# Kernel tuning notes

Measured on AMD Instinct MI355X. Metric: run time of the kernel, lower is better.

Reference implementation:

```python
import jax, jax.numpy as jnp
import numpy as np
from jax import lax

DIM = 2048
N_HEADS = 16
N_KV = 4
HEAD_DIM = DIM // N_HEADS  # 128
ROPE_BASE = 10000.0
SEQ = 4096
BSZ = 1


def bitlinear(x, W):
    # per-row abs-mean scale (detached), ternary round/clamp, straight-through blend
    s = lax.stop_gradient(jnp.clip(jnp.mean(jnp.abs(W), axis=1, keepdims=True), 1e-5, None))
    wt = jnp.clip(jnp.round(W / s), -1.0, 1.0)
    w = lax.stop_gradient(wt - W) + W  # straight-through
    return x @ (w * s).T


def rms_norm(x):
    eps = jnp.finfo(x.dtype).eps
    return x * lax.rsqrt(jnp.mean(x * x, axis=-1, keepdims=True) + eps)


def rope(x, cos, sin):
    half = x.shape[-1] // 2
    x1, x2 = x[..., :half], x[..., half:]
    return jnp.concatenate((x1 * cos + x2 * sin, -x1 * sin + x2 * cos), axis=-1)


def setup_inputs() -> dict:
    key = jax.random.key(0)
    ks = jax.random.split(key, 6)
    kv_dim = N_KV * HEAD_DIM
    return {
        "x": jax.random.normal(ks[0], (BSZ, SEQ, DIM), dtype=jnp.float32),
        "wq": jax.random.normal(ks[1], (DIM, DIM), dtype=jnp.float32) * 0.02,
        "wk": jax.random.normal(ks[2], (kv_dim, DIM), dtype=jnp.float32) * 0.02,
        "wv": jax.random.normal(ks[3], (kv_dim, DIM), dtype=jnp.float32) * 0.02,
        "wp": jax.random.normal(ks[4], (DIM, DIM), dtype=jnp.float32) * 0.02,
        "q_gain": jnp.ones((N_HEADS,), dtype=jnp.float32),
    }


def reference(x, wq, wk, wv, wp, q_gain):
    b, s, d = x.shape
    q = bitlinear(x, wq).reshape(b, s, N_HEADS, HEAD_DIM).transpose(0, 2, 1, 3)  # bhsd
    k = bitlinear(x, wk).reshape(b, s, N_KV, HEAD_DIM).transpose(0, 2, 1, 3)
    v = bitlinear(x, wv).reshape(b, s, N_KV, HEAD_DIM).transpose(0, 2, 1, 3)

    q = rms_norm(q)
    k = rms_norm(k)

    inv_freq = 1.0 / ROPE_BASE ** (jnp.arange(0, HEAD_DIM, 2, dtype=jnp.float32) / HEAD_DIM)
    t = jnp.arange(s, dtype=jnp.float32)
    freqs = jnp.outer(t, inv_freq)  # [s, hd/2]
    cos = jnp.cos(freqs)[None, None].astype(q.dtype)
    sin = jnp.sin(freqs)[None, None].astype(q.dtype)
    q = rope(q, cos, sin)
    k = rope(k, cos, sin)

    q = q * q_gain.astype(q.dtype)[None, :, None, None]

    groups = N_HEADS // N_KV
    k = jnp.repeat(k, groups, axis=1)  # GQA expand to [b, H, s, hd]
    v = jnp.repeat(v, groups, axis=1)

    scale = 1.0 / np.sqrt(HEAD_DIM)
    scores = jnp.einsum("bhqd,bhkd->bhqk", q, k) * scale
    causal = jnp.tril(jnp.ones((s, s), dtype=bool))
    scores = jnp.where(causal[None, None], scores, jnp.finfo(scores.dtype).min)
    attn = jax.nn.softmax(scores, axis=-1)
    y = jnp.einsum("bhqk,bhkd->bhqd", attn, v)

    y = y.transpose(0, 2, 1, 3).reshape(b, s, d)
    return bitlinear(y, wp)
```

## Files before the change

### kernel.cpp

```cpp
#include <hip/hip_runtime.h>
#include <math.h>

typedef unsigned short u16;
typedef short s16x8 __attribute__((ext_vector_type(8)));
typedef short s16x4 __attribute__((ext_vector_type(4)));
typedef float f32x4 __attribute__((ext_vector_type(4)));
typedef u16 u16x4 __attribute__((ext_vector_type(4)));

static constexpr size_t OFF_XB   = 0;
static constexpr size_t OFF_WQKV = 16777216;
static constexpr size_t OFF_WP   = 29360128;
static constexpr size_t OFF_QKV  = 37748736;
static constexpr size_t OFF_PART = 37748736 + 16777216;
static constexpr size_t OFF_KH   = 88080384;
static constexpr size_t OFF_VT   = 92274688;

__device__ __forceinline__ u16 f2bf(float f) {
  union { float f; unsigned u; } v; v.f = f;
  unsigned r = v.u + 0x7fffu + ((v.u >> 16) & 1u);
  return (u16)(r >> 16);
}

__device__ __forceinline__ void async16(const u16* g, u16* lds) {
  __builtin_amdgcn_global_load_lds(
      (const __attribute__((address_space(1))) void*)g,
      (__attribute__((address_space(3))) void*)lds, 16, 0, 0);
}

__global__ __launch_bounds__(256) void quant_rows(const float* __restrict__ W,
                                                  u16* __restrict__ out) {
  const int row = blockIdx.x, tid = threadIdx.x;
  const float* src = W + (size_t)row * 2048 + tid * 8;
  float4 a = *(const float4*)(src);
  float4 b = *(const float4*)(src + 4);
  float asum = fabsf(a.x)+fabsf(a.y)+fabsf(a.z)+fabsf(a.w)
             + fabsf(b.x)+fabsf(b.y)+fabsf(b.z)+fabsf(b.w);
  #pragma unroll
  for (int off = 1; off < 64; off <<= 1) asum += __shfl_xor(asum, off, 64);
  __shared__ float red[4];
  if ((tid & 63) == 0) red[tid >> 6] = asum;
  __syncthreads();
  float s = fmaxf((red[0]+red[1]+red[2]+red[3]) * (1.0f/2048.0f), 1e-5f);
  float v[8] = {a.x,a.y,a.z,a.w,b.x,b.y,b.z,b.w};
  u16* dst = out + (size_t)row * 2048 + tid * 8;
  #pragma unroll
  for (int i = 0; i < 8; i++) {
    float q = rintf(v[i] / s);
    q = fminf(fmaxf(q, -1.f), 1.f);
    dst[i] = f2bf(q * s);
  }
}

__global__ __launch_bounds__(256) void cvt_bf16(const float* __restrict__ in,
                                                u16* __restrict__ out) {
  size_t i = ((size_t)blockIdx.x * 256 + threadIdx.x) * 4;
  float4 v = *(const float4*)(in + i);
  u16x4 o;
  o.x = f2bf(v.x); o.y = f2bf(v.y); o.z = f2bf(v.z); o.w = f2bf(v.w);
  *(u16x4*)(out + i) = o;
}

__global__ __launch_bounds__(256) void gemm_bt(const u16* __restrict__ A,
                                               const u16* __restrict__ B,
                                               float* __restrict__ C,
                                               int M, int N, int K) {
  __shared__ u16 sA[128 * 32];
  __shared__ u16 sB[128 * 32];
  const int tid = threadIdx.x;
  const int lane = tid & 63;
  const int wid = tid >> 6;
  const int lr = lane & 15, lq = lane >> 4;
  const int wm = (wid >> 1) * 64, wn = (wid & 1) * 64;
  const size_t m0 = (size_t)blockIdx.y * 128, n0 = (size_t)blockIdx.x * 128;

  const int r0 = tid >> 2, c0 = (tid & 3) * 8;
  const u16* Ab0 = A + (m0 + r0) * (size_t)K + c0;
  const u16* Ab1 = A + (m0 + 64 + r0) * (size_t)K + c0;
  const u16* Bb0 = B + (n0 + r0) * (size_t)K + c0;
  const u16* Bb1 = B + (n0 + 64 + r0) * (size_t)K + c0;
  u16* sA0 = &sA[tid * 8];
  u16* sA1 = &sA[(256 + tid) * 8];
  u16* sB0 = &sB[tid * 8];
  u16* sB1 = &sB[(256 + tid) * 8];

  f32x4 acc[4][4] = {};

  for (int kt = 0; kt < K; kt += 32) {
    async16(Ab0 + kt, sA0);
    async16(Ab1 + kt, sA1);
    async16(Bb0 + kt, sB0);
    async16(Bb1 + kt, sB1);
    __syncthreads();
    s16x8 af[4], bf[4];
    #pragma unroll
    for (int mt = 0; mt < 4; mt++)
      af[mt] = *(const s16x8*)&sA[(wm + mt * 16 + lr) * 32 + lq * 8];
    #pragma unroll
    for (int nt = 0; nt < 4; nt++)
      bf[nt] = *(const s16x8*)&sB[(wn + nt * 16 + lr) * 32 + lq * 8];
    #pragma unroll
    for (int mt = 0; mt < 4; mt++)
      #pragma unroll
      for (int nt = 0; nt < 4; nt++)
        acc[mt][nt] = __builtin_amdgcn_mfma_f32_16x16x32_bf16(af[mt], bf[nt], acc[mt][nt], 0, 0, 0);
    __syncthreads();
  }
  #pragma unroll
  for (int mt = 0; mt < 4; mt++)
    #pragma unroll
    for (int nt = 0; nt < 4; nt++)
      #pragma unroll
      for (int r = 0; r < 4; r++) {
        size_t m = m0 + wm + mt * 16 + lq * 4 + r;
        size_t n = n0 + wn + nt * 16 + lr;
        C[m * (size_t)N + n] = acc[mt][nt][r];
      }
}

__global__ __launch_bounds__(256) void prep_qk(const float* __restrict__ qkv,
                                               const float* __restrict__ qgain,
                                               u16* __restrict__ Qh,
                                               u16* __restrict__ Kh) {
  const int s = blockIdx.y;
  const int j = blockIdx.x * 4 + (threadIdx.x >> 6);
  const int t = threadIdx.x & 63;
  const float* row = qkv + (size_t)s * 3072 + (size_t)j * 128;
  float x1 = row[t], x2 = row[t + 64];
  float ss = x1 * x1 + x2 * x2;
  #pragma unroll
  for (int off = 1; off < 64; off <<= 1) ss += __shfl_xor(ss, off, 64);
  float rn = rsqrtf(ss * (1.0f / 128.0f) + 1.1920929e-07f);
  float invf = exp2f(-(float)t * 0.20762050593048096f);
  float ang = (float)s * invf;
  float sn, c;
  sincosf(ang, &sn, &c);
  if (j < 16) {
    float g = qgain[j] * 0.12751738f;
    float q1 = x1 * rn, q2 = x2 * rn;
    float o1 = (q1 * c + q2 * sn) * g;
    float o2 = (-q1 * sn + q2 * c) * g;
    u16* dst = Qh + ((size_t)j * 4096 + s) * 128;
    dst[t] = f2bf(o1); dst[t + 64] = f2bf(o2);
  } else {
    float k1 = x1 * rn, k2 = x2 * rn;
    float o1 = k1 * c + k2 * sn;
    float o2 = -k1 * sn + k2 * c;
    u16* dst = Kh + ((size_t)(j - 16) * 4096 + s) * 128;
    dst[t] = f2bf(o1); dst[t + 64] = f2bf(o2);
  }
}

__global__ __launch_bounds__(256) void vtrans(const float* __restrict__ qkv,
                                              u16* __restrict__ Vtg) {
  __shared__ float tile[64][67];
  const int tid = threadIdx.x;
  const int s0 = blockIdx.y * 64;
  const int c0 = blockIdx.x * 64;
  #pragma unroll
  for (int it = 0; it < 4; it++) {
    int i = it * 256 + tid;
    int r = i >> 4, c = (i & 15) * 4;
    float4 v = *(const float4*)(qkv + (size_t)(s0 + r) * 3072 + 2560 + c0 + c);
    tile[r][c] = v.x; tile[r][c + 1] = v.y; tile[r][c + 2] = v.z; tile[r][c + 3] = v.w;
  }
  __syncthreads();
  #pragma unroll
  for (int it = 0; it < 2; it++) {
    int i = it * 256 + tid;
    int dl = i >> 3, sc = (i & 7) * 8;
    s16x8 ov;
    #pragma unroll
    for (int jj = 0; jj < 8; jj++) ov[jj] = (short)f2bf(tile[sc + jj][dl]);
    *(s16x8*)&Vtg[(size_t)(c0 + dl) * 4096 + s0 + sc] = ov;
  }
}

__global__ __launch_bounds__(256, 2) void attn(const u16* __restrict__ Q,
                                               const u16* __restrict__ Kh,
                                               const u16* __restrict__ Vt,
                                               u16* __restrict__ Y,
                                               float* __restrict__ Opart,
                                               float* __restrict__ MLpart) {
  const int tid = threadIdx.x, lane = tid & 63, wid = tid >> 6;
  const int lr = lane & 15, lq = lane >> 4;

  int rem = blockIdx.x, s = 32;
  for (;;) {
    int cnt = (s >= 17 ? 32 : 0) + (((s & 1) == 0) ? 16 : 0);
    if (rem < cnt) break;
    rem -= cnt; --s;
  }
  int qt, chunk, h, split;
  if (s >= 17 && rem < 32) { split = 1; qt = s - 1; chunk = rem >> 4; h = rem & 15; }
  else { split = 0; if (s >= 17) rem -= 32; qt = (s >> 1) - 1; chunk = 0; h = rem & 15; }
  const int t0 = split ? chunk * (qt + 1) : 0;
  const int t1 = split ? t0 + qt + 1 : 2 * qt + 2;
  const int kvh = h >> 2;
  const int qbase = qt * 128;

  __shared__ u16 sK[64][136];
  __shared__ u16 sVt[144][72];

  for (int i = tid; i < 16 * 72; i += 256) {
    int r = i / 72, c = i - r * 72;
    sVt[128 + r][c] = (r == 0) ? (u16)0x3F80 : (u16)0;
  }

  s16x8 qf[2][4];
  #pragma unroll
  for (int f = 0; f < 2; f++) {
    const u16* qp = Q + ((size_t)h * 4096 + qbase + wid * 32 + f * 16 + lr) * 128 + lq * 8;
    #pragma unroll
    for (int kc = 0; kc < 4; kc++) qf[f][kc] = *(const s16x8*)(qp + kc * 32);
  }

  f32x4 oacc[2][9] = {};
  float mrow[2] = {-1e30f, -1e30f};

  const u16* Kbase = Kh + (size_t)kvh * 4096 * 128;
  const u16* Vbase = Vt + (size_t)kvh * 128 * 4096;

  for (int t = t0; t < t1; ++t) {
    #pragma unroll
    for (int it = 0; it < 4; it++) {
      int idx = it * 256 + tid;
      int kr = idx >> 4, kc8 = (idx & 15) * 8;
      *(s16x8*)&sK[kr][kc8] = *(const s16x8*)(Kbase + (size_t)(t * 64 + kr) * 128 + kc8);
    }
    #pragma unroll
    for (int it = 0; it < 4; it++) {
      int idx = it * 256 + tid;
      int vd = idx >> 3, vc = (idx & 7) * 8;
      s16x8 v = *(const s16x8*)(Vbase + (size_t)vd * 4096 + t * 64 + vc);
      int g0 = ((vc >> 2) & 3) * 16 + (vc >> 4) * 4;
      int g1 = ((((vc >> 2) & 3) + 1)) * 16 + (vc >> 4) * 4;
      s16x4 lo = {v[0], v[1], v[2], v[3]};
      s16x4 hi = {v[4], v[5], v[6], v[7]};
      *(s16x4*)&sVt[vd][g0] = lo;
      *(s16x4*)&sVt[vd][g1] = hi;
    }
    __syncthreads();

    f32x4 sacc[2][4] = {};
    #pragma unroll
    for (int nt = 0; nt < 4; nt++)
      #pragma unroll
      for (int kc = 0; kc < 4; kc++) {
        s16x8 kf = *(const s16x8*)&sK[nt * 16 + lr][kc * 32 + lq * 8];
        sacc[0][nt] = __builtin_amdgcn_mfma_f32_16x16x32_bf16(kf, qf[0][kc], sacc[0][nt], 0, 0, 0);
        sacc[1][nt] = __builtin_amdgcn_mfma_f32_16x16x32_bf16(kf, qf[1][kc], sacc[1][nt], 0, 0, 0);
      }

    if (t >= 2 * qt) {
      #pragma unroll
      for (int f = 0; f < 2; f++) {
        int qg = qbase + wid * 32 + f * 16 + lr;
        #pragma unroll
        for (int nt = 0; nt < 4; nt++) {
          int kv0 = t * 64 + nt * 16 + lq * 4;
          #pragma unroll
          for (int r = 0; r < 4; r++)
            if (kv0 + r > qg) sacc[f][nt][r] = -1e30f;
        }
      }
    }

    float mx[2];
    #pragma unroll
    for (int f = 0; f < 2; f++) {
      float m01 = fmaxf(fmaxf(sacc[f][0][0], sacc[f][0][1]), fmaxf(sacc[f][0][2], sacc[f][0][3]));
      float m23 = fmaxf(fmaxf(sacc[f][1][0], sacc[f][1][1]), fmaxf(sacc[f][1][2], sacc[f][1][3]));
      float m45 = fmaxf(fmaxf(sacc[f][2][0], sacc[f][2][1]), fmaxf(sacc[f][2][2], sacc[f][2][3]));
      float m67 = fmaxf(fmaxf(sacc[f][3][0], sacc[f][3][1]), fmaxf(sacc[f][3][2], sacc[f][3][3]));
      mx[f] = fmaxf(fmaxf(m01, m23), fmaxf(m45, m67));
      mx[f] = fmaxf(mx[f], __shfl_xor(mx[f], 16, 64));
      mx[f] = fmaxf(mx[f], __shfl_xor(mx[f], 32, 64));
    }

    bool grow = (mx[0] > mrow[0]) || (mx[1] > mrow[1]);
    if (__any(grow)) {
      #pragma unroll
      for (int f = 0; f < 2; f++) {
        float mn = fmaxf(mrow[f], mx[f]);
        float al = exp2f(mrow[f] - mn);
        mrow[f] = mn;
        #pragma unroll
        for (int dt = 0; dt < 9; dt++)
          #pragma unroll
          for (int r = 0; r < 4; r++) oacc[f][dt][r] *= al;
      }
    }

    s16x4 pf[2][4];
    #pragma unroll
    for (int f = 0; f < 2; f++)
      #pragma unroll
      for (int nt = 0; nt < 4; nt++)
        #pragma unroll
        for (int r = 0; r < 4; r++) {
          union { float fv; unsigned u; } pu;
          pu.fv = exp2f(sacc[f][nt][r] - mrow[f]);
          pf[f][nt][r] = (short)(pu.u >> 16);
        }

    #pragma unroll
    for (int dt = 0; dt < 9; dt++) {
      s16x8 v01 = *(const s16x8*)&sVt[dt * 16 + lr][lq * 16];
      s16x8 v23 = *(const s16x8*)&sVt[dt * 16 + lr][lq * 16 + 8];
      s16x4 vf0 = {v01[0], v01[1], v01[2], v01[3]};
      s16x4 vf1 = {v01[4], v01[5], v01[6], v01[7]};
      s16x4 vf2 = {v23[0], v23[1], v23[2], v23[3]};
      s16x4 vf3 = {v23[4], v23[5], v23[6], v23[7]};
      #pragma unroll
      for (int f = 0; f < 2; f++) {
        oacc[f][dt] = __builtin_amdgcn_mfma_f32_16x16x16bf16_1k(vf0, pf[f][0], oacc[f][dt], 0, 0, 0);
        oacc[f][dt] = __builtin_amdgcn_mfma_f32_16x16x16bf16_1k(vf1, pf[f][1], oacc[f][dt], 0, 0, 0);
        oacc[f][dt] = __builtin_amdgcn_mfma_f32_16x16x16bf16_1k(vf2, pf[f][2], oacc[f][dt], 0, 0, 0);
        oacc[f][dt] = __builtin_amdgcn_mfma_f32_16x16x16bf16_1k(vf3, pf[f][3], oacc[f][dt], 0, 0, 0);
      }
    }
    __syncthreads();
  }

  if (split) {
    const int pidx = ((qt - 16) * 16 + h) * 2 + chunk;
    float* Op = Opart + (size_t)pidx * 16384;
    #pragma unroll
    for (int f = 0; f < 2; f++) {
      int row = wid * 32 + f * 16 + lr;
      #pragma unroll
      for (int dt = 0; dt < 8; dt++)
        *(f32x4*)&Op[row * 128 + dt * 16 + lq * 4] = oacc[f][dt];
    }
    if (lq == 0) {
      #pragma unroll
      for (int f = 0; f < 2; f++) {
        int row = wid * 32 + f * 16 + lr;
        MLpart[(size_t)pidx * 256 + row * 2]     = mrow[f];
        MLpart[(size_t)pidx * 256 + row * 2 + 1] = oacc[f][8][0];
      }
    }
  } else {
    #pragma unroll
    for (int f = 0; f < 2; f++) {
      float lv = __shfl(oacc[f][8][0], lr, 64);
      float linv = 1.0f / lv;
      int qg = qbase + wid * 32 + f * 16 + lr;
      #pragma unroll
      for (int dt = 0; dt < 8; dt++) {
        u16 tmp[4];
        #pragma unroll
        for (int r = 0; r < 4; r++) tmp[r] = f2bf(oacc[f][dt][r] * linv);
        *(s16x4*)&Y[(size_t)qg * 2048 + h * 128 + dt * 16 + lq * 4] = *(s16x4*)tmp;
      }
    }
  }
}

__global__ __launch_bounds__(256) void combine(const float* __restrict__ Op,
                                               const float* __restrict__ ML,
                                               u16* __restrict__ Y) {
  const int blk = blockIdx.x;
  const int qt16 = blk >> 4, h = blk & 15;
  const int p0 = blk * 2, p1 = p0 + 1;
  const int tid = threadIdx.x;
  const int row = tid >> 1, half = (tid & 1) * 64;
  float m0 = ML[(size_t)p0 * 256 + row * 2], l0 = ML[(size_t)p0 * 256 + row * 2 + 1];
  float m1 = ML[(size_t)p1 * 256 + row * 2], l1 = ML[(size_t)p1 * 256 + row * 2 + 1];
  float m = fmaxf(m0, m1);
  float w0 = exp2f(m0 - m), w1 = exp2f(m1 - m);
  float inv = 1.0f / (l0 * w0 + l1 * w1);
  w0 *= inv; w1 *= inv;
  const float* o0 = Op + (size_t)p0 * 16384 + row * 128 + half;
  const float* o1 = Op + (size_t)p1 * 16384 + row * 128 + half;
  size_t q = (size_t)(qt16 + 16) * 128 + row;
  u16* dst = Y + q * 2048 + h * 128 + half;
  #pragma unroll
  for (int c = 0; c < 64; c += 8) {
    float4 a0 = *(const float4*)(o0 + c), b0 = *(const float4*)(o0 + c + 4);
    float4 a1 = *(const float4*)(o1 + c), b1 = *(const float4*)(o1 + c + 4);
    u16 tmp[8];
    tmp[0] = f2bf(a0.x * w0 + a1.x * w1);
    tmp[1] = f2bf(a0.y * w0 + a1.y * w1);
    tmp[2] = f2bf(a0.z * w0 + a1.z * w1);
    tmp[3] = f2bf(a0.w * w0 + a1.w * w1);
    tmp[4] = f2bf(b0.x * w0 + b1.x * w1);
    tmp[5] = f2bf(b0.y * w0 + b1.y * w1);
    tmp[6] = f2bf(b0.z * w0 + b1.z * w1);
    tmp[7] = f2bf(b0.w * w0 + b1.w * w1);
    *(s16x8*)(dst + c) = *(s16x8*)tmp;
  }
}

extern "C" void kernel_launch(void* const* d_in, const int* in_sizes, int n_in,
                              void* d_out, int out_size, void* d_ws, size_t ws_size,
                              hipStream_t stream) {
  const float* x  = (const float*)d_in[0];
  const float* wq = (const float*)d_in[1];
  const float* wk = (const float*)d_in[2];
  const float* wv = (const float*)d_in[3];
  const float* wp = (const float*)d_in[4];
  const float* qg = (const float*)d_in[5];
  float* out = (float*)d_out;
  char* ws = (char*)d_ws;

  u16*   XB    = (u16*)(ws + OFF_XB);
  u16*   WQKV  = (u16*)(ws + OFF_WQKV);
  u16*   WP    = (u16*)(ws + OFF_WP);
  float* QKV   = (float*)(ws + OFF_QKV);
  u16*   QH    = XB;
  u16*   KH    = (u16*)(ws + OFF_KH);
  u16*   VT    = (u16*)(ws + OFF_VT);
  u16*   Yb    = (u16*)(ws + OFF_QKV);
  float* OPART = (float*)(ws + OFF_PART);
  float* MLP   = (float*)(ws + OFF_WQKV);

  quant_rows<<<2048, 256, 0, stream>>>(wq, WQKV);
  quant_rows<<<512,  256, 0, stream>>>(wk, WQKV + (size_t)2048 * 2048);
  quant_rows<<<512,  256, 0, stream>>>(wv, WQKV + (size_t)2560 * 2048);
  quant_rows<<<2048, 256, 0, stream>>>(wp, WP);
  cvt_bf16<<<8192, 256, 0, stream>>>(x, XB);
  gemm_bt<<<dim3(24, 32), 256, 0, stream>>>(XB, WQKV, QKV, 4096, 3072, 2048);
  prep_qk<<<dim3(5, 4096), 256, 0, stream>>>(QKV, qg, QH, KH);
  vtrans<<<dim3(8, 64), 256, 0, stream>>>(QKV, VT);
  attn<<<768, 256, 0, stream>>>(QH, KH, VT, Yb, OPART, MLP);
  combine<<<256, 256, 0, stream>>>(OPART, MLP, Yb);
  gemm_bt<<<dim3(16, 32), 256, 0, stream>>>(Yb, WP, out, 4096, 2048, 2048);
}
```

Measured before the change: 430.2 us.

## Split every query tile into two KV chunks and track row sums in registers

The attention grid is now uniform. Every query tile for every head is split into two equal KV chunks, giving 1024 blocks, and all results go through the combine kernel. Before, only the longer tiles were split and the rest used a packed schedule. The softmax denominator is now a per-row register sum with shuffle reductions instead of an extra ones-row MFMA tile, which drops the ninth output tile. Partial outputs are stored as bf16 rather than fp32 to halve partial traffic, at the cost of an extra rounding step and a combine pass over all tiles, including the short ones that previously wrote their output directly.

```diff
diff --git a/kernel.cpp b/kernel.cpp
--- a/kernel.cpp
+++ b/kernel.cpp
@@ -11,7 +11,7 @@
 static constexpr size_t OFF_WQKV = 16777216;
 static constexpr size_t OFF_WP   = 29360128;
 static constexpr size_t OFF_QKV  = 37748736;
-static constexpr size_t OFF_PART = 37748736 + 16777216;
+static constexpr size_t OFF_Y    = 37748736 + 33554432;
 static constexpr size_t OFF_KH   = 88080384;
 static constexpr size_t OFF_VT   = 92274688;
 
@@ -19,6 +19,11 @@
   union { float f; unsigned u; } v; v.f = f;
   unsigned r = v.u + 0x7fffu + ((v.u >> 16) & 1u);
   return (u16)(r >> 16);
+}
+
+__device__ __forceinline__ float bf2f(u16 b) {
+  union { unsigned u; float f; } v; v.u = ((unsigned)b) << 16;
+  return v.f;
 }
 
 __device__ __forceinline__ void async16(const u16* g, u16* lds) {
@@ -178,33 +183,23 @@
 __global__ __launch_bounds__(256, 2) void attn(const u16* __restrict__ Q,
                                                const u16* __restrict__ Kh,
                                                const u16* __restrict__ Vt,
-                                               u16* __restrict__ Y,
-                                               float* __restrict__ Opart,
+                                               u16* __restrict__ Opart,
                                                float* __restrict__ MLpart) {
   const int tid = threadIdx.x, lane = tid & 63, wid = tid >> 6;
   const int lr = lane & 15, lq = lane >> 4;
 
-  int rem = blockIdx.x, s = 32;
-  for (;;) {
-    int cnt = (s >= 17 ? 32 : 0) + (((s & 1) == 0) ? 16 : 0);
-    if (rem < cnt) break;
-    rem -= cnt; --s;
-  }
-  int qt, chunk, h, split;
-  if (s >= 17 && rem < 32) { split = 1; qt = s - 1; chunk = rem >> 4; h = rem & 15; }
-  else { split = 0; if (s >= 17) rem -= 32; qt = (s >> 1) - 1; chunk = 0; h = rem & 15; }
-  const int t0 = split ? chunk * (qt + 1) : 0;
-  const int t1 = split ? t0 + qt + 1 : 2 * qt + 2;
+  const int b = blockIdx.x;
+  const int h = b & 15;
+  const int p = b >> 4;
+  const int qt = 31 - (p >> 1);
+  const int chunk = p & 1;
+  const int t0 = chunk * (qt + 1);
+  const int t1 = t0 + qt + 1;
   const int kvh = h >> 2;
   const int qbase = qt * 128;
 
   __shared__ u16 sK[64][136];
-  __shared__ u16 sVt[144][72];
-
-  for (int i = tid; i < 16 * 72; i += 256) {
-    int r = i / 72, c = i - r * 72;
-    sVt[128 + r][c] = (r == 0) ? (u16)0x3F80 : (u16)0;
-  }
+  __shared__ u16 sVt[128][72];
 
   s16x8 qf[2][4];
   #pragma unroll
@@ -214,8 +209,9 @@
     for (int kc = 0; kc < 4; kc++) qf[f][kc] = *(const s16x8*)(qp + kc * 32);
   }
 
-  f32x4 oacc[2][9] = {};
+  f32x4 oacc[2][8] = {};
   float mrow[2] = {-1e30f, -1e30f};
+  float lrow[2] = {0.f, 0.f};
 
   const u16* Kbase = Kh + (size_t)kvh * 4096 * 128;
   const u16* Vbase = Vt + (size_t)kvh * 128 * 4096;
@@ -233,7 +229,7 @@
       int vd = idx >> 3, vc = (idx & 7) * 8;
       s16x8 v = *(const s16x8*)(Vbase + (size_t)vd * 4096 + t * 64 + vc);
       int g0 = ((vc >> 2) & 3) * 16 + (vc >> 4) * 4;
-      int g1 = ((((vc >> 2) & 3) + 1)) * 16 + (vc >> 4) * 4;
+      int g1 = (((vc >> 2) & 3) + 1) * 16 + (vc >> 4) * 4;
       s16x4 lo = {v[0], v[1], v[2], v[3]};
       s16x4 hi = {v[4], v[5], v[6], v[7]};
       *(s16x4*)&sVt[vd][g0] = lo;
@@ -284,14 +280,16 @@
         float mn = fmaxf(mrow[f], mx[f]);
         float al = exp2f(mrow[f] - mn);
         mrow[f] = mn;
+        lrow[f] *= al;
         #pragma unroll
-        for (int dt = 0; dt < 9; dt++)
+        for (int dt = 0; dt < 8; dt++)
           #pragma unroll
           for (int r = 0; r < 4; r++) oacc[f][dt][r] *= al;
       }
     }
 
     s16x4 pf[2][4];
+    float rsum[2] = {0.f, 0.f};
     #pragma unroll
     for (int f = 0; f < 2; f++)
       #pragma unroll
@@ -300,11 +298,18 @@
         for (int r = 0; r < 4; r++) {
           union { float fv; unsigned u; } pu;
           pu.fv = exp2f(sacc[f][nt][r] - mrow[f]);
+          rsum[f] += pu.fv;
           pf[f][nt][r] = (short)(pu.u >> 16);
         }
-
-    #pragma unroll
-    for (int dt = 0; dt < 9; dt++) {
+    #pragma unroll
+    for (int f = 0; f < 2; f++) {
+      rsum[f] += __shfl_xor(rsum[f], 16, 64);
+      rsum[f] += __shfl_xor(rsum[f], 32, 64);
+      lrow[f] += rsum[f];
+    }
+
+    #pragma unroll
+    for (int dt = 0; dt < 8; dt++) {
       s16x8 v01 = *(const s16x8*)&sVt[dt * 16 + lr][lq * 16];
       s16x8 v23 = *(const s16x8*)&sVt[dt * 16 + lr][lq * 16 + 8];
       s16x4 vf0 = {v01[0], v01[1], v01[2], v01[3]};
@@ -322,72 +327,55 @@
     __syncthreads();
   }
 
-  if (split) {
-    const int pidx = ((qt - 16) * 16 + h) * 2 + chunk;
-    float* Op = Opart + (size_t)pidx * 16384;
+  u16* Op = Opart + (size_t)b * 16384;
+  #pragma unroll
+  for (int f = 0; f < 2; f++) {
+    int row = wid * 32 + f * 16 + lr;
+    #pragma unroll
+    for (int dt = 0; dt < 8; dt++) {
+      u16 tmp[4];
+      #pragma unroll
+      for (int r = 0; r < 4; r++) tmp[r] = f2bf(oacc[f][dt][r]);
+      *(s16x4*)&Op[row * 128 + dt * 16 + lq * 4] = *(s16x4*)tmp;
+    }
+  }
+  if (lq == 0) {
     #pragma unroll
     for (int f = 0; f < 2; f++) {
       int row = wid * 32 + f * 16 + lr;
-      #pragma unroll
-      for (int dt = 0; dt < 8; dt++)
-        *(f32x4*)&Op[row * 128 + dt * 16 + lq * 4] = oacc[f][dt];
-    }
-    if (lq == 0) {
-      #pragma unroll
-      for (int f = 0; f < 2; f++) {
-        int row = wid * 32 + f * 16 + lr;
-        MLpart[(size_t)pidx * 256 + row * 2]     = mrow[f];
-        MLpart[(size_t)pidx * 256 + row * 2 + 1] = oacc[f][8][0];
-      }
-    }
-  } else {
-    #pragma unroll
-    for (int f = 0; f < 2; f++) {
-      float lv = __shfl(oacc[f][8][0], lr, 64);
-      float linv = 1.0f / lv;
-      int qg = qbase + wid * 32 + f * 16 + lr;
-      #pragma unroll
-      for (int dt = 0; dt < 8; dt++) {
-        u16 tmp[4];
-        #pragma unroll
-        for (int r = 0; r < 4; r++) tmp[r] = f2bf(oacc[f][dt][r] * linv);
-        *(s16x4*)&Y[(size_t)qg * 2048 + h * 128 + dt * 16 + lq * 4] = *(s16x4*)tmp;
-      }
-    }
-  }
-}
-
-__global__ __launch_bounds__(256) void combine(const float* __restrict__ Op,
+      MLpart[(size_t)b * 256 + row * 2]     = mrow[f];
+      MLpart[(size_t)b * 256 + row * 2 + 1] = lrow[f];
+    }
+  }
+}
+
+__global__ __launch_bounds__(256) void combine(const u16* __restrict__ Op,
                                                const float* __restrict__ ML,
                                                u16* __restrict__ Y) {
   const int blk = blockIdx.x;
-  const int qt16 = blk >> 4, h = blk & 15;
-  const int p0 = blk * 2, p1 = p0 + 1;
+  const int qtc = blk >> 4, h = blk & 15;
+  const int qt = 31 - qtc;
+  const int b0 = (qtc * 2) * 16 + h, b1 = b0 + 16;
   const int tid = threadIdx.x;
   const int row = tid >> 1, half = (tid & 1) * 64;
-  float m0 = ML[(size_t)p0 * 256 + row * 2], l0 = ML[(size_t)p0 * 256 + row * 2 + 1];
-  float m1 = ML[(size_t)p1 * 256 + row * 2], l1 = ML[(size_t)p1 * 256 + row * 2 + 1];
+  float m0 = ML[(size_t)b0 * 256 + row * 2], l0 = ML[(size_t)b0 * 256 + row * 2 + 1];
+  float m1 = ML[(size_t)b1 * 256 + row * 2], l1 = ML[(size_t)b1 * 256 + row * 2 + 1];
   float m = fmaxf(m0, m1);
   float w0 = exp2f(m0 - m), w1 = exp2f(m1 - m);
   float inv = 1.0f / (l0 * w0 + l1 * w1);
   w0 *= inv; w1 *= inv;
-  const float* o0 = Op + (size_t)p0 * 16384 + row * 128 + half;
-  const float* o1 = Op + (size_t)p1 * 16384 + row * 128 + half;
-  size_t q = (size_t)(qt16 + 16) * 128 + row;
+  const u16* o0 = Op + (size_t)b0 * 16384 + row * 128 + half;
+  const u16* o1 = Op + (size_t)b1 * 16384 + row * 128 + half;
+  size_t q = (size_t)qt * 128 + row;
   u16* dst = Y + q * 2048 + h * 128 + half;
   #pragma unroll
   for (int c = 0; c < 64; c += 8) {
-    float4 a0 = *(const float4*)(o0 + c), b0 = *(const float4*)(o0 + c + 4);
-    float4 a1 = *(const float4*)(o1 + c), b1 = *(const float4*)(o1 + c + 4);
+    s16x8 a0 = *(const s16x8*)(o0 + c);
+    s16x8 a1 = *(const s16x8*)(o1 + c);
     u16 tmp[8];
-    tmp[0] = f2bf(a0.x * w0 + a1.x * w1);
-    tmp[1] = f2bf(a0.y * w0 + a1.y * w1);
-    tmp[2] = f2bf(a0.z * w0 + a1.z * w1);
-    tmp[3] = f2bf(a0.w * w0 + a1.w * w1);
-    tmp[4] = f2bf(b0.x * w0 + b1.x * w1);
-    tmp[5] = f2bf(b0.y * w0 + b1.y * w1);
-    tmp[6] = f2bf(b0.z * w0 + b1.z * w1);
-    tmp[7] = f2bf(b0.w * w0 + b1.w * w1);
+    #pragma unroll
+    for (int jj = 0; jj < 8; jj++)
+      tmp[jj] = f2bf(bf2f((u16)a0[jj]) * w0 + bf2f((u16)a1[jj]) * w1);
     *(s16x8*)(dst + c) = *(s16x8*)tmp;
   }
 }
@@ -411,8 +399,8 @@
   u16*   QH    = XB;
   u16*   KH    = (u16*)(ws + OFF_KH);
   u16*   VT    = (u16*)(ws + OFF_VT);
-  u16*   Yb    = (u16*)(ws + OFF_QKV);
-  float* OPART = (float*)(ws + OFF_PART);
+  u16*   OPART = (u16*)(ws + OFF_QKV);
+  u16*   Yb    = (u16*)(ws + OFF_Y);
   float* MLP   = (float*)(ws + OFF_WQKV);
 
   quant_rows<<<2048, 256, 0, stream>>>(wq, WQKV);
@@ -423,7 +411,7 @@
   gemm_bt<<<dim3(24, 32), 256, 0, stream>>>(XB, WQKV, QKV, 4096, 3072, 2048);
   prep_qk<<<dim3(5, 4096), 256, 0, stream>>>(QKV, qg, QH, KH);
   vtrans<<<dim3(8, 64), 256, 0, stream>>>(QKV, VT);
-  attn<<<768, 256, 0, stream>>>(QH, KH, VT, Yb, OPART, MLP);
-  combine<<<256, 256, 0, stream>>>(OPART, MLP, Yb);
+  attn<<<1024, 256, 0, stream>>>(QH, KH, VT, OPART, MLP);
+  combine<<<512, 256, 0, stream>>>(OPART, MLP, Yb);
   gemm_bt<<<dim3(16, 32), 256, 0, stream>>>(Yb, WP, out, 4096, 2048, 2048);
 }
```

Measured after the change: 419.9 us. 1.02x faster.
